# Kernel tuning notes

Measured on AMD Instinct MI355X. Metric: run time of the kernel, lower is better.

Reference implementation:

```python
import jax, jax.numpy as jnp
import numpy as np

N_SAMPLES = 32768   # exp.n_samples = 2**15
N_FRAMES = 128      # exp.n_frames = n_samples // 256
N_EVENTS = 16
MODEL_DIM = 128
N_FREQS = 16        # 2*16 + 1 = 33 pos-encoding features
POS_DIM = 2 * N_FREQS + 1


def pos_encoded(n_frames, n_freqs):
    # linear position in [-pi, pi] plus sin/cos at geometrically spaced freqs
    x = np.linspace(-np.pi, np.pi, n_frames, dtype=np.float32)[:, None]
    feats = [x]
    for i in range(n_freqs):
        feats.append(np.sin((2.0 ** i) * x))
        feats.append(np.cos((2.0 ** i) * x))
    return jnp.asarray(np.concatenate(feats, axis=-1))  # (n_frames, 33)


def hard_softmax_st(x):
    # softmax -> one-hot at argmax (value forced to exactly 1.0), straight-through backward
    sm = jax.nn.softmax(x, axis=-1)
    onehot = jax.nn.one_hot(jnp.argmax(sm, axis=-1), x.shape[-1], dtype=x.dtype)
    return sm + jax.lax.stop_gradient(onehot - sm)


def fft_convolve(env, tf):
    n = env.shape[-1]
    env = jnp.pad(env, ((0, 0), (0, 0), (0, n)))
    tf = jnp.pad(tf, ((0, 0), (0, 0), (0, n)))
    spec = jnp.fft.rfft(env, axis=-1, norm='ortho') * jnp.fft.rfft(tf, axis=-1, norm='ortho')
    return jnp.fft.irfft(spec, axis=-1, norm='ortho')[..., :n]


def setup_inputs() -> dict:
    key = jax.random.key(0)
    k1, k2, k3, k4, k5 = jax.random.split(key, 5)
    B = 32
    time_latent = jax.random.normal(k1, (B * N_EVENTS, MODEL_DIM), jnp.float32)
    stems = jax.random.normal(k2, (B, N_EVENTS, N_SAMPLES), jnp.float32)
    targets = jax.random.normal(k3, (B, N_EVENTS, N_SAMPLES), jnp.float32)
    lim = 1.0 / np.sqrt(MODEL_DIM)
    W = jax.random.uniform(k4, (MODEL_DIM, POS_DIM), jnp.float32, -lim, lim)
    b = jax.random.uniform(k5, (POS_DIM,), jnp.float32, -lim, lim)
    return {"time_latent": time_latent, "stems": stems, "targets": targets, "W": W, "b": b}


def reference(time_latent, stems, targets, W, b):
    # to_pos linear projection: (B*E, 128) -> (B*E, 33)
    p = time_latent @ W + b
    p = p / (jnp.linalg.norm(p, axis=-1, keepdims=True) + 1e-8)
    pos = pos_encoded(N_FRAMES, N_FREQS)
    pos = pos / (jnp.linalg.norm(pos, axis=-1, keepdims=True) + 1e-8)
    sim = p @ pos.T                      # (B*E, n_frames)
    sm = hard_softmax_st(sim)            # one-hot forward, softmax backward
    step = N_SAMPLES // N_FRAMES         # 256
    sparse = jnp.zeros((p.shape[0], N_SAMPLES), p.dtype).at[:, ::step].set(sm)
    sparse = sparse.reshape(-1, N_EVENTS, N_SAMPLES)  # (B, 16, 32768)
    return fft_convolve(sparse, stems)
```

## Files before the change

### kernel.cpp

```cpp
#include <hip/hip_runtime.h>
#include <math.h>

#define N_SAMPLES 32768
#define N_FRAMES  128
#define N_EVENTS  16
#define MODEL_DIM 128
#define N_FREQS   16
#define POS_DIM   33
#define N_ROWS    512
#define SPLIT     8

#define WS_P_OFF 17408

__global__ __launch_bounds__(128) void setup_kernel(
    const float* __restrict__ tl,
    const float* __restrict__ W,
    const float* __restrict__ b,
    float* __restrict__ pos_hat,
    float* __restrict__ p_out)
{
    int bid = blockIdx.x;
    int t = threadIdx.x;

    if (bid < N_FRAMES) {
        int f = bid;
        __shared__ float s_feat[POS_DIM];
        __shared__ float s_inv;

        double step = (2.0 * M_PI) / 127.0;
        double xd = -M_PI + (double)f * step;
        if (f == N_FRAMES - 1) xd = M_PI;
        float x = (float)xd;

        if (t < POS_DIM) {
            float v;
            if (t == 0) {
                v = x;
            } else {
                int i = (t - 1) >> 1;
                double arg = ldexp((double)x, i);
                v = (t & 1) ? (float)sin(arg) : (float)cos(arg);
            }
            s_feat[t] = v;
        }
        __syncthreads();

        if (t == 0) {
            double nrm = 0.0;
            for (int k = 0; k < POS_DIM; ++k)
                nrm += (double)s_feat[k] * (double)s_feat[k];
            s_inv = 1.0f / ((float)sqrt(nrm) + 1e-8f);
        }
        __syncthreads();

        if (t < POS_DIM) pos_hat[f * POS_DIM + t] = s_feat[t] * s_inv;
    } else {
        int row = bid - N_FRAMES;
        __shared__ float s_tl[MODEL_DIM];

        s_tl[t] = tl[(size_t)row * MODEL_DIM + t];
        __syncthreads();

        if (t < POS_DIM) {
            double acc = (double)b[t];
            for (int k = 0; k < MODEL_DIM; ++k)
                acc += (double)s_tl[k] * (double)W[k * POS_DIM + t];
            p_out[row * POS_DIM + t] = (float)acc;
        }
    }
}

__global__ __launch_bounds__(256) void shift_kernel(
    const float* __restrict__ p,
    const float* __restrict__ pos_hat,
    const float* __restrict__ stems,
    float*       __restrict__ out)
{
    __shared__ float  s_p[POS_DIM];
    __shared__ double sv[N_FRAMES];
    __shared__ int    si[N_FRAMES];
    __shared__ int    s_d;

    int row = blockIdx.y;
    int t = threadIdx.x;

    if (t < POS_DIM) s_p[t] = p[row * POS_DIM + t];
    __syncthreads();

    if (t < N_FRAMES) {
        double s = 0.0;
        for (int j = 0; j < POS_DIM; ++j)
            s += (double)s_p[j] * (double)pos_hat[t * POS_DIM + j];
        sv[t] = s;
        si[t] = t;
    }
    __syncthreads();

    for (int off = 64; off > 0; off >>= 1) {
        if (t < off) {
            double ov = sv[t + off];
            int    oi = si[t + off];
            if (ov > sv[t] || (ov == sv[t] && oi < si[t])) {
                sv[t] = ov;
                si[t] = oi;
            }
        }
        __syncthreads();
    }
    if (t == 0) s_d = si[0] * (N_SAMPLES / N_FRAMES);
    __syncthreads();

    int d = s_d;
    const float4* src = (const float4*)(stems + (size_t)row * N_SAMPLES);
    float4*       dst = (float4*)(out + (size_t)row * N_SAMPLES);
    const float sc = 1.0f / 256.0f;

    int base = blockIdx.x * (N_SAMPLES / SPLIT);
#pragma unroll
    for (int it = 0; it < (N_SAMPLES / SPLIT) / (256 * 4); ++it) {
        int tt = base + (it * 256 + t) * 4;
        float4 v;
        if (tt >= d) {
            v = src[(tt - d) >> 2];
            v.x *= sc; v.y *= sc; v.z *= sc; v.w *= sc;
        } else {
            v = make_float4(0.f, 0.f, 0.f, 0.f);
        }
        dst[tt >> 2] = v;
    }
}

extern "C" void kernel_launch(void* const* d_in, const int* in_sizes, int n_in,
                              void* d_out, int out_size, void* d_ws, size_t ws_size,
                              hipStream_t stream) {
    const float* tl    = (const float*)d_in[0];
    const float* stems = (const float*)d_in[1];
    const float* W     = (const float*)d_in[3];
    const float* b     = (const float*)d_in[4];
    float* out = (float*)d_out;

    float* pos_hat = (float*)d_ws;
    float* p       = (float*)((char*)d_ws + WS_P_OFF);

    setup_kernel<<<N_FRAMES + N_ROWS, 128, 0, stream>>>(tl, W, b, pos_hat, p);
    shift_kernel<<<dim3(SPLIT, N_ROWS), 256, 0, stream>>>(p, pos_hat, stems, out);
}
```

Before: 175.3 us.

## Split argmax into its own kernel and make shift a pure copy

Moves the per-row similarity and argmax into a separate kernel that writes shift offsets to workspace. The shift kernel becomes a lightweight copy with one float4 per thread over many more blocks. This removes the argmax being recomputed in each of the 8 blocks per row, and lets the copy run with high occupancy and no reduction or syncs before the copy starts. The cost is an extra kernel launch and a small global round trip for the offsets.

```diff
diff --git a/kernel.cpp b/kernel.cpp
--- a/kernel.cpp
+++ b/kernel.cpp
@@ -8,9 +8,9 @@
 #define N_FREQS   16
 #define POS_DIM   33
 #define N_ROWS    512
-#define SPLIT     8
 
 #define WS_P_OFF 17408
+#define WS_D_OFF 85504
 
 __global__ __launch_bounds__(128) void setup_kernel(
     const float* __restrict__ tl,
@@ -70,30 +70,26 @@
     }
 }
 
-__global__ __launch_bounds__(256) void shift_kernel(
+__global__ __launch_bounds__(128) void argmax_kernel(
     const float* __restrict__ p,
     const float* __restrict__ pos_hat,
-    const float* __restrict__ stems,
-    float*       __restrict__ out)
+    int* __restrict__ dout)
 {
     __shared__ float  s_p[POS_DIM];
     __shared__ double sv[N_FRAMES];
     __shared__ int    si[N_FRAMES];
-    __shared__ int    s_d;
 
-    int row = blockIdx.y;
+    int row = blockIdx.x;
     int t = threadIdx.x;
 
     if (t < POS_DIM) s_p[t] = p[row * POS_DIM + t];
     __syncthreads();
 
-    if (t < N_FRAMES) {
-        double s = 0.0;
-        for (int j = 0; j < POS_DIM; ++j)
-            s += (double)s_p[j] * (double)pos_hat[t * POS_DIM + j];
-        sv[t] = s;
-        si[t] = t;
-    }
+    double s = 0.0;
+    for (int j = 0; j < POS_DIM; ++j)
+        s += (double)s_p[j] * (double)pos_hat[t * POS_DIM + j];
+    sv[t] = s;
+    si[t] = t;
     __syncthreads();
 
     for (int off = 64; off > 0; off >>= 1) {
@@ -107,27 +103,30 @@
         }
         __syncthreads();
     }
-    if (t == 0) s_d = si[0] * (N_SAMPLES / N_FRAMES);
-    __syncthreads();
+    if (t == 0) dout[row] = si[0] * (N_SAMPLES / N_FRAMES);
+}
 
-    int d = s_d;
+__global__ __launch_bounds__(256) void shift_kernel(
+    const float* __restrict__ stems,
+    const int*   __restrict__ dvals,
+    float*       __restrict__ out)
+{
+    int row = blockIdx.y;
+    int t = (blockIdx.x * 256 + threadIdx.x) * 4;
+    int d = dvals[row];
+
     const float4* src = (const float4*)(stems + (size_t)row * N_SAMPLES);
     float4*       dst = (float4*)(out + (size_t)row * N_SAMPLES);
-    const float sc = 1.0f / 256.0f;
 
-    int base = blockIdx.x * (N_SAMPLES / SPLIT);
-#pragma unroll
-    for (int it = 0; it < (N_SAMPLES / SPLIT) / (256 * 4); ++it) {
-        int tt = base + (it * 256 + t) * 4;
-        float4 v;
-        if (tt >= d) {
-            v = src[(tt - d) >> 2];
-            v.x *= sc; v.y *= sc; v.z *= sc; v.w *= sc;
-        } else {
-            v = make_float4(0.f, 0.f, 0.f, 0.f);
-        }
-        dst[tt >> 2] = v;
+    float4 v;
+    if (t >= d) {
+        v = src[(t - d) >> 2];
+        const float sc = 1.0f / 256.0f;
+        v.x *= sc; v.y *= sc; v.z *= sc; v.w *= sc;
+    } else {
+        v = make_float4(0.f, 0.f, 0.f, 0.f);
     }
+    dst[t >> 2] = v;
 }
 
 extern "C" void kernel_launch(void* const* d_in, const int* in_sizes, int n_in,
@@ -141,7 +140,9 @@
 
     float* pos_hat = (float*)d_ws;
     float* p       = (float*)((char*)d_ws + WS_P_OFF);
+    int*   dvals   = (int*)((char*)d_ws + WS_D_OFF);
 
     setup_kernel<<<N_FRAMES + N_ROWS, 128, 0, stream>>>(tl, W, b, pos_hat, p);
-    shift_kernel<<<dim3(SPLIT, N_ROWS), 256, 0, stream>>>(p, pos_hat, stems, out);
+    argmax_kernel<<<N_ROWS, 128, 0, stream>>>(p, pos_hat, dvals);
+    shift_kernel<<<dim3(N_SAMPLES / (256 * 4), N_ROWS), 256, 0, stream>>>(stems, dvals, out);
 }
```

Result: faster. 169.6 us (-3.2%).
